# Kernel tuning notes

Measured on AMD Instinct MI355X. Metric: run time of the kernel, lower is better.

The kernel has to match this reference:

```python
import jax, jax.numpy as jnp
import numpy as np

B, L, E, H = 1, 4096, 1024, 16
D = E // H
EPS = 1e-6


def setup_inputs() -> dict:
    key = jax.random.key(0)
    k1, k2, k3 = jax.random.split(key, 3)
    # fan-in scaled init to keep activations sane
    x = jax.random.normal(k1, (B, L, E), dtype=jnp.float32)
    qkv_w = jax.random.normal(k2, (E, 3 * E), dtype=jnp.float32) / np.sqrt(E)
    qkv_b = jnp.zeros((3 * E,), dtype=jnp.float32)
    out_w = jax.random.normal(k3, (E, E), dtype=jnp.float32) / np.sqrt(E)
    out_b = jnp.zeros((E,), dtype=jnp.float32)
    return {"x": x, "qkv_w": qkv_w, "qkv_b": qkv_b, "out_w": out_w, "out_b": out_b}


def reference(x, qkv_w, qkv_b, out_w, out_b):
    b, l, e = x.shape
    qkv = x @ qkv_w + qkv_b                      # (B, L, 3E)
    q, k, v = jnp.split(qkv, 3, axis=-1)
    # (B, L, E) -> (B, H, L, D)
    q = q.reshape(b, l, H, D).transpose(0, 2, 1, 3)
    k = k.reshape(b, l, H, D).transpose(0, 2, 1, 3)
    v = v.reshape(b, l, H, D).transpose(0, 2, 1, 3)
    q_prime = jax.nn.elu(q) + 1.0
    k_prime = jax.nn.elu(k) + 1.0
    # cumulative sum of per-position outer products k'_l v_l^T : (B,H,L,D,D)
    kv_prod = jnp.einsum('bhld,bhle->bhlde', k_prime, v)
    kv_cumsum = jnp.cumsum(kv_prod, axis=2)
    context = jnp.einsum('bhld,bhlde->bhle', q_prime, kv_cumsum)  # (B,H,L,D)
    k_cumsum = jnp.cumsum(k_prime, axis=2)                        # (B,H,L,D)
    norm = jnp.einsum('bhld,bhld->bhl', q_prime, k_cumsum)        # (B,H,L)
    output = context / (norm[..., None] + EPS)
    output = output.transpose(0, 2, 1, 3).reshape(b, l, e)
    return output @ out_w + out_b
```

## Files before the change

kernel.cpp:

```cpp
#include <hip/hip_runtime.h>
#include <cstddef>
#include <cstdint>

#define L_SEQ 4096
#define EMB   1024
#define NH    16
#define HD    64
#define N3    3072
#define CHUNK 64
#define NCHUNK 64
#define EPS 1e-6f

typedef __attribute__((ext_vector_type(8))) short   bf16x8;
typedef __attribute__((ext_vector_type(4))) short   bf16x4;
typedef __attribute__((ext_vector_type(4))) float   floatx4;

#define AS1 __attribute__((address_space(1)))
#define AS3 __attribute__((address_space(3)))

__device__ __forceinline__ void gload_lds16(const void* g, void* l) {
    __builtin_amdgcn_global_load_lds((AS1 const unsigned int*)g,
                                     (AS3 unsigned int*)l, 16, 0, 0);
}

__device__ __forceinline__ short f2bf(float f) {
    union { float f; unsigned u; } a; a.f = f;
    unsigned r = a.u + 0x7fffu + ((a.u >> 16) & 1u);
    return (short)(r >> 16);
}
__device__ __forceinline__ float bf2f(short s) {
    union { unsigned u; float f; } a; a.u = ((unsigned)(unsigned short)s) << 16;
    return a.f;
}

__device__ __forceinline__ void transpose_tile(const float* __restrict__ W,
                                               short* __restrict__ WT,
                                               int K, int N, int bx, int by,
                                               float (*t)[65], int tid)
{
    const int r  = tid >> 4;
    const int c4 = (tid & 15) << 2;
#pragma unroll
    for (int s = 0; s < 4; ++s) {
        const int k = r + s * 16;
        const floatx4 v = *(const floatx4*)&W[(size_t)(by * 64 + k) * N + bx * 64 + c4];
        t[k][c4 + 0] = v[0]; t[k][c4 + 1] = v[1];
        t[k][c4 + 2] = v[2]; t[k][c4 + 3] = v[3];
    }
    __syncthreads();
#pragma unroll
    for (int s = 0; s < 4; ++s) {
        const int n = r + s * 16;
        bf16x4 o;
        o[0] = f2bf(t[c4 + 0][n]); o[1] = f2bf(t[c4 + 1][n]);
        o[2] = f2bf(t[c4 + 2][n]); o[3] = f2bf(t[c4 + 3][n]);
        *(bf16x4*)&WT[(size_t)(bx * 64 + n) * K + by * 64 + c4] = o;
    }
}

__global__ __launch_bounds__(256)
void prep(const float* __restrict__ x, short* __restrict__ xb,
          const float* __restrict__ qkv_w, short* __restrict__ qwt,
          const float* __restrict__ out_w, short* __restrict__ owt)
{
    __shared__ float t[64][65];
    const int b = blockIdx.x;
    const int tid = threadIdx.x;
    if (b < 2048) {
        const int i = b * 256 + tid;
        const floatx4 a = *(const floatx4*)(x + (size_t)i * 8);
        const floatx4 c = *(const floatx4*)(x + (size_t)i * 8 + 4);
        bf16x8 o;
        o[0] = f2bf(a[0]); o[1] = f2bf(a[1]); o[2] = f2bf(a[2]); o[3] = f2bf(a[3]);
        o[4] = f2bf(c[0]); o[5] = f2bf(c[1]); o[6] = f2bf(c[2]); o[7] = f2bf(c[3]);
        *(bf16x8*)(xb + (size_t)i * 8) = o;
    } else if (b < 2048 + 768) {
        const int u = b - 2048;
        transpose_tile(qkv_w, qwt, EMB, N3, u % 48, u / 48, t, tid);
    } else {
        const int u = b - 2816;
        transpose_tile(out_w, owt, EMB, EMB, u & 15, u >> 4, t, tid);
    }
}

#define CST 136

__global__ __launch_bounds__(256)
void mfma_gemm_qkv(const short* __restrict__ A, const short* __restrict__ BT,
                   const float* __restrict__ bias,
                   short* __restrict__ OQ, short* __restrict__ OK,
                   short* __restrict__ OV, int N, int K)
{
    __shared__ __align__(16) short smem[128 * CST];
    short* pan[4] = { smem, smem + 4096, smem + 8192, smem + 12288 };
    const int tid  = threadIdx.x;
    const int lane = tid & 63;
    const int wave = tid >> 6;
    const int wm = (wave >> 1) * 64;
    const int wn = (wave & 1) * 64;
    const int bx = blockIdx.x;
    const int by = blockIdx.y;
    const int frow = lane & 15;
    const int quad = lane >> 4;
    const int fko  = quad << 3;

    const short* Ab = A  + (size_t)(by * 128) * K;
    const short* Bb = BT + (size_t)(bx * 128) * K;

    floatx4 acc[4][4] = {};

    for (int k0 = 0; k0 < K; k0 += 64) {
#pragma unroll
        for (int p = 0; p < 2; ++p) {
            const int kp = k0 + p * 32;
#pragma unroll
            for (int q = 0; q < 2; ++q) {
                const int ia = q * 256 + tid;
                const int row = ia >> 2;
                const int kc  = (ia & 3) << 3;
                gload_lds16(Ab + (size_t)row * K + kp + kc, &pan[p * 2 + 0][ia << 3]);
                gload_lds16(Bb + (size_t)row * K + kp + kc, &pan[p * 2 + 1][ia << 3]);
            }
        }
        __syncthreads();
#pragma unroll
        for (int p = 0; p < 2; ++p) {
            bf16x8 af[4], bfv[4];
#pragma unroll
            for (int mi = 0; mi < 4; ++mi)
                af[mi] = *(const bf16x8*)&pan[p * 2 + 0][(wm + mi * 16 + frow) * 32 + fko];
#pragma unroll
            for (int ni = 0; ni < 4; ++ni)
                bfv[ni] = *(const bf16x8*)&pan[p * 2 + 1][(wn + ni * 16 + frow) * 32 + fko];
#pragma unroll
            for (int mi = 0; mi < 4; ++mi)
#pragma unroll
                for (int ni = 0; ni < 4; ++ni)
                    acc[mi][ni] = __builtin_amdgcn_mfma_f32_16x16x32_bf16(
                        af[mi], bfv[ni], acc[mi][ni], 0, 0, 0);
        }
        __syncthreads();
    }

    const int rq = quad << 2;
#pragma unroll
    for (int ni = 0; ni < 4; ++ni) {
        const int n = bx * 128 + wn + ni * 16 + frow;
        const float bv = bias[n];
        const bool do_elu = (n >> 10) < 2;
#pragma unroll
        for (int mi = 0; mi < 4; ++mi)
#pragma unroll
            for (int r = 0; r < 4; ++r) {
                float v = acc[mi][ni][r] + bv;
                if (do_elu) v = (v > 0.f) ? (v + 1.f) : __expf(v);
                smem[(wm + mi * 16 + rq + r) * CST + wn + ni * 16 + frow] = f2bf(v);
            }
    }
    __syncthreads();
#pragma unroll
    for (int t = 0; t < 8; ++t) {
        const int idx = t * 256 + tid;
        const int mm = idx >> 4;
        const int c8 = (idx & 15) << 3;
        const bf16x8 val = *(const bf16x8*)&smem[mm * CST + c8];
        const int n0 = bx * 128 + c8;
        const int rsel = n0 >> 10;
        const int h  = (n0 & 1023) >> 6;
        const int d  = n0 & 63;
        short* base = (rsel == 0) ? OQ : (rsel == 1 ? OK : OV);
        *(bf16x8*)&base[((size_t)(h * L_SEQ + by * 128 + mm)) * HD + d] = val;
    }
}

__global__ __launch_bounds__(256)
void mfma_gemm_out(const short* __restrict__ A, const short* __restrict__ BT,
                   const float* __restrict__ bias, float* __restrict__ OF,
                   int N, int K)
{
    __shared__ __align__(16) short smem[12288];
    short* pan[4] = { smem, smem + 2048, smem + 6144, smem + 8192 };
    const int tid  = threadIdx.x;
    const int lane = tid & 63;
    const int wave = tid >> 6;
    const int wm = (wave >> 1) * 32;
    const int wn = (wave & 1) * 64;
    const int bx = blockIdx.x;
    const int by = blockIdx.y;
    const int frow = lane & 15;
    const int quad = lane >> 4;
    const int fko  = quad << 3;

    const short* Ab = A  + (size_t)(by * 64) * K;
    const short* Bb = BT + (size_t)(bx * 128) * K;

    floatx4 acc[2][4] = {};

    for (int k0 = 0; k0 < K; k0 += 64) {
#pragma unroll
        for (int p = 0; p < 2; ++p) {
            const int kp = k0 + p * 32;
            {
                const int row = tid >> 2;
                const int kc  = (tid & 3) << 3;
                gload_lds16(Ab + (size_t)row * K + kp + kc, &pan[p * 2 + 0][tid << 3]);
            }
#pragma unroll
            for (int q = 0; q < 2; ++q) {
                const int ib = q * 256 + tid;
                const int row = ib >> 2;
                const int kc  = (ib & 3) << 3;
                gload_lds16(Bb + (size_t)row * K + kp + kc, &pan[p * 2 + 1][ib << 3]);
            }
        }
        __syncthreads();
#pragma unroll
        for (int p = 0; p < 2; ++p) {
            bf16x8 af[2], bfv[4];
#pragma unroll
            for (int mi = 0; mi < 2; ++mi)
                af[mi] = *(const bf16x8*)&pan[p * 2 + 0][(wm + mi * 16 + frow) * 32 + fko];
#pragma unroll
            for (int ni = 0; ni < 4; ++ni)
                bfv[ni] = *(const bf16x8*)&pan[p * 2 + 1][(wn + ni * 16 + frow) * 32 + fko];
#pragma unroll
            for (int mi = 0; mi < 2; ++mi)
#pragma unroll
                for (int ni = 0; ni < 4; ++ni)
                    acc[mi][ni] = __builtin_amdgcn_mfma_f32_16x16x32_bf16(
                        af[mi], bfv[ni], acc[mi][ni], 0, 0, 0);
        }
        __syncthreads();
    }

    const int rq = quad << 2;
#pragma unroll
    for (int ni = 0; ni < 4; ++ni) {
        const int n = bx * 128 + wn + ni * 16 + frow;
        const float bv = bias[n];
#pragma unroll
        for (int mi = 0; mi < 2; ++mi)
#pragma unroll
            for (int r = 0; r < 4; ++r) {
                const int m = by * 64 + wm + mi * 16 + rq + r;
                OF[(size_t)m * N + n] = acc[mi][ni][r] + bv;
            }
    }
}

#define SP 72

__global__ __launch_bounds__(256, 4)
void chunk_state(const short* __restrict__ Kb, const short* __restrict__ Vb,
                 short* __restrict__ ScTb, float* __restrict__ zc)
{
    __shared__ __align__(16) short Vt[64 * SP];
    __shared__ __align__(16) short Kt[64 * SP];
    const int c = blockIdx.x, h = blockIdx.y;
    const int tid = threadIdx.x, lane = tid & 63, wave = tid >> 6;
    const int frow = lane & 15;
    const int quad = lane >> 4;
    const int fko  = quad << 3;
    const int wm   = wave << 4;
    const short* Kg = Kb + ((size_t)h * L_SEQ + (size_t)c * CHUNK) * HD;
    const short* Vg = Vb + ((size_t)h * L_SEQ + (size_t)c * CHUNK) * HD;

#pragma unroll
    for (int q = 0; q < 2; ++q) {
        const int idx = q * 256 + tid;
        const int l = idx >> 3, c8 = (idx & 7) << 3;
        const bf16x8 vv = *(const bf16x8*)&Vg[l * 64 + c8];
        const bf16x8 kk = *(const bf16x8*)&Kg[l * 64 + c8];
#pragma unroll
        for (int j = 0; j < 8; ++j) {
            Vt[(c8 + j) * SP + l] = vv[j];
            Kt[(c8 + j) * SP + l] = kk[j];
        }
    }
    __syncthreads();

    const bf16x8 af0 = *(const bf16x8*)&Vt[(wm + frow) * SP + fko];
    const bf16x8 af1 = *(const bf16x8*)&Vt[(wm + frow) * SP + 32 + fko];

    floatx4 acc[4] = {};
#pragma unroll
    for (int n = 0; n < 4; ++n) {
        const bf16x8 kf0 = *(const bf16x8*)&Kt[(n * 16 + frow) * SP + fko];
        const bf16x8 kf1 = *(const bf16x8*)&Kt[(n * 16 + frow) * SP + 32 + fko];
        acc[n] = __builtin_amdgcn_mfma_f32_16x16x32_bf16(af0, kf0, acc[n], 0, 0, 0);
        acc[n] = __builtin_amdgcn_mfma_f32_16x16x32_bf16(af1, kf1, acc[n], 0, 0, 0);
    }

    short* Sout = ScTb + (size_t)(h * NCHUNK + c) * 4096;
#pragma unroll
    for (int n = 0; n < 4; ++n)
#pragma unroll
        for (int r = 0; r < 4; ++r) {
            const int e = wm + quad * 4 + r;
            const int d = n * 16 + frow;
            Sout[e * 64 + d] = f2bf(acc[n][r]);
        }

    if (wave == 0) {
        bf16x8 ones;
#pragma unroll
        for (int j = 0; j < 8; ++j) ones[j] = (short)0x3F80;
        floatx4 zacc[4] = {};
#pragma unroll
        for (int n = 0; n < 4; ++n) {
            const bf16x8 kf0 = *(const bf16x8*)&Kt[(n * 16 + frow) * SP + fko];
            const bf16x8 kf1 = *(const bf16x8*)&Kt[(n * 16 + frow) * SP + 32 + fko];
            zacc[n] = __builtin_amdgcn_mfma_f32_16x16x32_bf16(ones, kf0, zacc[n], 0, 0, 0);
            zacc[n] = __builtin_amdgcn_mfma_f32_16x16x32_bf16(ones, kf1, zacc[n], 0, 0, 0);
        }
        if (quad == 0) {
#pragma unroll
            for (int n = 0; n < 4; ++n)
                zc[(size_t)(h * NCHUNK + c) * 64 + n * 16 + frow] = zacc[n][0];
        }
    }
}

__global__ __launch_bounds__(256)
void prefix_scan(const short* __restrict__ ScTb, const float* __restrict__ zc,
                 short* __restrict__ S0b)
{
    const int g = blockIdx.x * 256 + threadIdx.x;
    const int h  = g >> 12;
    const int ed = g & 4095;
    const int e  = ed >> 6;
    const int d  = ed & 63;
    const short* src = ScTb + (size_t)h * NCHUNK * 4096 + ed;
    float run = 0.f;
    for (int cb = 0; cb < NCHUNK; cb += 8) {
        short v[8];
#pragma unroll
        for (int u = 0; u < 8; ++u) v[u] = src[(size_t)(cb + u) * 4096];
#pragma unroll
        for (int u = 0; u < 8; ++u) {
            S0b[((size_t)((h * NCHUNK + cb + u) * 65 + e)) * 64 + d] = f2bf(run);
            run += bf2f(v[u]);
        }
    }
    if (g < NH * HD) {
        const int h2 = g >> 6, d2 = g & 63;
        float rz = 0.f;
        for (int cb = 0; cb < NCHUNK; cb += 8) {
            float w[8];
#pragma unroll
            for (int u = 0; u < 8; ++u)
                w[u] = zc[((size_t)(h2 * NCHUNK + cb + u)) * HD + d2];
#pragma unroll
            for (int u = 0; u < 8; ++u) {
                S0b[((size_t)((h2 * NCHUNK + cb + u) * 65 + 64)) * 64 + d2] = f2bf(rz);
                rz += w[u];
            }
        }
    }
}

__global__ __launch_bounds__(256)
void chunk_attn(const short* __restrict__ Qb, const short* __restrict__ Kb,
                const short* __restrict__ Vb, const short* __restrict__ S0b,
                short* __restrict__ attn)
{
    __shared__ __align__(16) short Vs[65 * SP];
    __shared__ __align__(16) short As[64 * SP];
    const int c = blockIdx.x, h = blockIdx.y;
    const int tid = threadIdx.x, lane = tid & 63, wave = tid >> 6;
    const size_t rb = ((size_t)h * L_SEQ + (size_t)c * CHUNK) * HD;
    const short* Qg = Qb + rb;
    const short* Kg = Kb + rb;
    const short* Vg = Vb + rb;
    const short* Sg = S0b + (size_t)(h * NCHUNK + c) * 65 * 64;

#pragma unroll
    for (int q = 0; q < 2; ++q) {
        const int idx = q * 256 + tid;
        const int row = idx >> 3, c8 = (idx & 7) << 3;
        const bf16x8 vv = *(const bf16x8*)&Vg[row * 64 + c8];
#pragma unroll
        for (int j = 0; j < 8; ++j) Vs[(c8 + j) * SP + row] = vv[j];
    }
    if (tid < 64) Vs[64 * SP + tid] = (short)0x3F80;
    __syncthreads();

    const int frow = lane & 15;
    const int quad = lane >> 4;
    const int fko  = quad << 3;
    const int wm   = wave << 4;

    const bf16x8 qf0 = *(const bf16x8*)&Qg[(wm + frow) * 64 + fko];
    const bf16x8 qf1 = *(const bf16x8*)&Qg[(wm + frow) * 64 + 32 + fko];

    floatx4 sacc[4] = {};
#pragma unroll
    for (int n = 0; n < 4; ++n) {
        const bf16x8 kf0 = *(const bf16x8*)&Kg[(n * 16 + frow) * 64 + fko];
        const bf16x8 kf1 = *(const bf16x8*)&Kg[(n * 16 + frow) * 64 + 32 + fko];
        sacc[n] = __builtin_amdgcn_mfma_f32_16x16x32_bf16(qf0, kf0, sacc[n], 0, 0, 0);
        sacc[n] = __builtin_amdgcn_mfma_f32_16x16x32_bf16(qf1, kf1, sacc[n], 0, 0, 0);
    }
#pragma unroll
    for (int n = 0; n < 4; ++n)
#pragma unroll
        for (int r = 0; r < 4; ++r) {
            const int i = wm + quad * 4 + r;
            const int j = n * 16 + frow;
            As[i * SP + j] = (j <= i) ? f2bf(sacc[n][r]) : (short)0;
        }
    const bf16x8 af0 = *(const bf16x8*)&As[(wm + frow) * SP + fko];
    const bf16x8 af1 = *(const bf16x8*)&As[(wm + frow) * SP + 32 + fko];

    floatx4 oacc[5] = {};
#pragma unroll
    for (int n = 0; n < 4; ++n) {
        const bf16x8 vf0 = *(const bf16x8*)&Vs[(n * 16 + frow) * SP + fko];
        const bf16x8 vf1 = *(const bf16x8*)&Vs[(n * 16 + frow) * SP + 32 + fko];
        oacc[n] = __builtin_amdgcn_mfma_f32_16x16x32_bf16(af0, vf0, oacc[n], 0, 0, 0);
        oacc[n] = __builtin_amdgcn_mfma_f32_16x16x32_bf16(af1, vf1, oacc[n], 0, 0, 0);
        const bf16x8 sf0 = *(const bf16x8*)&Sg[(n * 16 + frow) * 64 + fko];
        const bf16x8 sf1 = *(const bf16x8*)&Sg[(n * 16 + frow) * 64 + 32 + fko];
        oacc[n] = __builtin_amdgcn_mfma_f32_16x16x32_bf16(qf0, sf0, oacc[n], 0, 0, 0);
        oacc[n] = __builtin_amdgcn_mfma_f32_16x16x32_bf16(qf1, sf1, oacc[n], 0, 0, 0);
    }
    {
        const bf16x8 vf0 = *(const bf16x8*)&Vs[64 * SP + fko];
        const bf16x8 vf1 = *(const bf16x8*)&Vs[64 * SP + 32 + fko];
        oacc[4] = __builtin_amdgcn_mfma_f32_16x16x32_bf16(af0, vf0, oacc[4], 0, 0, 0);
        oacc[4] = __builtin_amdgcn_mfma_f32_16x16x32_bf16(af1, vf1, oacc[4], 0, 0, 0);
        const bf16x8 sf0 = *(const bf16x8*)&Sg[64 * 64 + fko];
        const bf16x8 sf1 = *(const bf16x8*)&Sg[64 * 64 + 32 + fko];
        oacc[4] = __builtin_amdgcn_mfma_f32_16x16x32_bf16(qf0, sf0, oacc[4], 0, 0, 0);
        oacc[4] = __builtin_amdgcn_mfma_f32_16x16x32_bf16(qf1, sf1, oacc[4], 0, 0, 0);
    }
#pragma unroll
    for (int r = 0; r < 4; ++r) {
        const float norm = __shfl(oacc[4][r], lane & 48) + EPS;
        const float inv = 1.f / norm;
        const int i = wm + quad * 4 + r;
#pragma unroll
        for (int n = 0; n < 4; ++n)
            As[i * SP + n * 16 + frow] = f2bf(oacc[n][r] * inv);
    }
    __syncthreads();
#pragma unroll
    for (int t = 0; t < 2; ++t) {
        const int idx = t * 256 + tid;
        const int row = idx >> 3, c8 = (idx & 7) << 3;
        *(bf16x8*)&attn[(size_t)(c * CHUNK + row) * EMB + h * HD + c8] =
            *(const bf16x8*)&As[row * SP + c8];
    }
}

extern "C" void kernel_launch(void* const* d_in, const int* in_sizes, int n_in,
                              void* d_out, int out_size, void* d_ws, size_t ws_size,
                              hipStream_t stream)
{
    const float* x     = (const float*)d_in[0];
    const float* qkv_w = (const float*)d_in[1];
    const float* qkv_b = (const float*)d_in[2];
    const float* out_w = (const float*)d_in[3];
    const float* out_b = (const float*)d_in[4];
    float* out = (float*)d_out;

    short* ws    = (short*)d_ws;
    short* Qb    = ws;
    short* Kb    = Qb + 4194304;
    short* Vb    = Kb + 4194304;
    short* xb    = Vb + 4194304;
    short* qwt   = xb + 4194304;
    short* owt   = qwt + 3145728;
    short* attnb = owt + 1048576;
    short* ScTb  = attnb + 4194304;
    short* S0b   = ScTb + 4194304;
    float* zc    = (float*)(S0b + 4259840);

    prep<<<dim3(3072), 256, 0, stream>>>(x, xb, qkv_w, qwt, out_w, owt);
    mfma_gemm_qkv<<<dim3(N3 / 128, L_SEQ / 128), 256, 0, stream>>>(
        xb, qwt, qkv_b, Qb, Kb, Vb, N3, EMB);
    chunk_state<<<dim3(NCHUNK, NH), 256, 0, stream>>>(Kb, Vb, ScTb, zc);
    prefix_scan<<<dim3((NH * 4096) / 256), 256, 0, stream>>>(ScTb, zc, S0b);
    chunk_attn<<<dim3(NCHUNK, NH), 256, 0, stream>>>(Qb, Kb, Vb, S0b, attnb);
    mfma_gemm_out<<<dim3(EMB / 128, L_SEQ / 64), 256, 0, stream>>>(
        attnb, owt, out_b, out, EMB, EMB);
}
```

Measured before the change: 166.3 us.

## Rewrite QKV GEMM as 256x256 tile with swizzled LDS and phased prefetch pipeline

Replaces the 128x128, 256-thread QKV GEMM with a 256x256, 512-thread kernel that uses 128KB of LDS, an XOR-swizzled layout to avoid bank conflicts, and an 8-phase schedule. Each phase overlaps global-to-LDS staging of the next K slices with MFMA work, using explicit barriers, waitcnt and setprio. The aim is higher data reuse per tile and hidden load latency. The trade-off is only 12x16=192 blocks on a large GPU, which risks underfilling the CUs, plus heavy LDS use and fragile manual synchronisation.

Result: no change. 168.3 us (+1.2%).

```diff
diff --git a/kernel.cpp b/kernel.cpp
--- a/kernel.cpp
+++ b/kernel.cpp
@@ -83,94 +83,141 @@
     }
 }
 
-#define CST 136
-
-__global__ __launch_bounds__(256)
-void mfma_gemm_qkv(const short* __restrict__ A, const short* __restrict__ BT,
-                   const float* __restrict__ bias,
-                   short* __restrict__ OQ, short* __restrict__ OK,
-                   short* __restrict__ OV, int N, int K)
-{
-    __shared__ __align__(16) short smem[128 * CST];
-    short* pan[4] = { smem, smem + 4096, smem + 8192, smem + 12288 };
+#define MFMA16 __builtin_amdgcn_mfma_f32_16x16x32_bf16
+
+__global__ __launch_bounds__(512, 2)
+void mfma_gemm_qkv256(const short* __restrict__ A, const short* __restrict__ BT,
+                      const float* __restrict__ bias,
+                      short* __restrict__ OQ, short* __restrict__ OK,
+                      short* __restrict__ OV)
+{
+    __shared__ __align__(16) short lds[65536];
     const int tid  = threadIdx.x;
     const int lane = tid & 63;
     const int wave = tid >> 6;
-    const int wm = (wave >> 1) * 64;
-    const int wn = (wave & 1) * 64;
+    const int wr   = wave >> 2;
+    const int wc   = wave & 3;
+    const int frow = lane & 15;
+    const int quad = lane >> 4;
+    const int q8   = quad * 8;
     const int bx = blockIdx.x;
     const int by = blockIdx.y;
-    const int frow = lane & 15;
-    const int quad = lane >> 4;
-    const int fko  = quad << 3;
-
-    const short* Ab = A  + (size_t)(by * 128) * K;
-    const short* Bb = BT + (size_t)(bx * 128) * K;
-
-    floatx4 acc[4][4] = {};
-
-    for (int k0 = 0; k0 < K; k0 += 64) {
-#pragma unroll
-        for (int p = 0; p < 2; ++p) {
-            const int kp = k0 + p * 32;
-#pragma unroll
-            for (int q = 0; q < 2; ++q) {
-                const int ia = q * 256 + tid;
-                const int row = ia >> 2;
-                const int kc  = (ia & 3) << 3;
-                gload_lds16(Ab + (size_t)row * K + kp + kc, &pan[p * 2 + 0][ia << 3]);
-                gload_lds16(Bb + (size_t)row * K + kp + kc, &pan[p * 2 + 1][ia << 3]);
-            }
-        }
-        __syncthreads();
-#pragma unroll
-        for (int p = 0; p < 2; ++p) {
-            bf16x8 af[4], bfv[4];
-#pragma unroll
-            for (int mi = 0; mi < 4; ++mi)
-                af[mi] = *(const bf16x8*)&pan[p * 2 + 0][(wm + mi * 16 + frow) * 32 + fko];
-#pragma unroll
-            for (int ni = 0; ni < 4; ++ni)
-                bfv[ni] = *(const bf16x8*)&pan[p * 2 + 1][(wn + ni * 16 + frow) * 32 + fko];
-#pragma unroll
-            for (int mi = 0; mi < 4; ++mi)
-#pragma unroll
-                for (int ni = 0; ni < 4; ++ni)
-                    acc[mi][ni] = __builtin_amdgcn_mfma_f32_16x16x32_bf16(
-                        af[mi], bfv[ni], acc[mi][ni], 0, 0, 0);
-        }
-        __syncthreads();
-    }
-
-    const int rq = quad << 2;
+
+    const short* Ab = A  + (size_t)(by * 256) * 1024;
+    const short* Bb = BT + (size_t)(bx * 256) * 1024;
+
+    const int trow = tid >> 3;
+    const int ccol = (tid & 7) * 8;
+    const int scol = ccol ^ ((trow & 12) << 2);
+    const int sx = (frow & 12) << 2;
+    const int wcb = wc * 64 + frow;
+
+#define STG(LBASE, GPTR) do {                                               \
+        const short* g_ = (GPTR);                                           \
+        _Pragma("unroll")                                                   \
+        for (int j_ = 0; j_ < 2; ++j_) {                                    \
+            const int r_ = j_ * 64 + trow;                                  \
+            gload_lds16(g_ + (size_t)r_ * 1024 + scol,                      \
+                        &lds[(LBASE) + r_ * 64 + ccol]);                    \
+        }                                                                   \
+    } while (0)
+
+#define LDA(BASE, R, KS) \
+    (*(const bf16x8*)&lds[(BASE) + (R) * 64 + ((((KS) * 32) + q8) ^ sx)])
+
+    floatx4 acc[8][4] = {};
+    bf16x8  bq[4][2];
+
+#define PHASE(ABASE, BBASE, QD, RDB, VM, ...) do {                          \
+        const int Rr_ = wr * 128 + (QD) * 32 + frow;                        \
+        bf16x8 a0_ = LDA((ABASE), Rr_,      0);                             \
+        bf16x8 a1_ = LDA((ABASE), Rr_,      1);                             \
+        bf16x8 a2_ = LDA((ABASE), Rr_ + 16, 0);                             \
+        bf16x8 a3_ = LDA((ABASE), Rr_ + 16, 1);                             \
+        if (RDB) {                                                          \
+            _Pragma("unroll")                                               \
+            for (int ni_ = 0; ni_ < 4; ++ni_) {                             \
+                bq[ni_][0] = LDA((BBASE), wcb + ni_ * 16, 0);               \
+                bq[ni_][1] = LDA((BBASE), wcb + ni_ * 16, 1);               \
+            }                                                               \
+        }                                                                   \
+        __VA_ARGS__;                                                        \
+        __builtin_amdgcn_sched_barrier(0);                                  \
+        __builtin_amdgcn_s_barrier();                                       \
+        asm volatile("s_waitcnt lgkmcnt(0)" ::: "memory");                  \
+        __builtin_amdgcn_sched_barrier(0);                                  \
+        __builtin_amdgcn_s_setprio(1);                                      \
+        _Pragma("unroll")                                                   \
+        for (int ni_ = 0; ni_ < 4; ++ni_) {                                 \
+            acc[2*(QD)  ][ni_] = MFMA16(a0_, bq[ni_][0], acc[2*(QD)  ][ni_], 0,0,0); \
+            acc[2*(QD)  ][ni_] = MFMA16(a1_, bq[ni_][1], acc[2*(QD)  ][ni_], 0,0,0); \
+            acc[2*(QD)+1][ni_] = MFMA16(a2_, bq[ni_][0], acc[2*(QD)+1][ni_], 0,0,0); \
+            acc[2*(QD)+1][ni_] = MFMA16(a3_, bq[ni_][1], acc[2*(QD)+1][ni_], 0,0,0); \
+        }                                                                   \
+        __builtin_amdgcn_s_setprio(0);                                      \
+        if (VM) asm volatile("s_waitcnt vmcnt(4)" ::: "memory");            \
+        __builtin_amdgcn_s_barrier();                                       \
+        __builtin_amdgcn_sched_barrier(0);                                  \
+    } while (0)
+
+    STG(0,     Ab);
+    STG(8192,  Ab + 131072);
+    STG(16384, Bb);
+    STG(24576, Bb + 131072);
+    STG(49152, Bb + 64);
+    STG(57344, Bb + 131072 + 64);
+    asm volatile("s_waitcnt vmcnt(4)" ::: "memory");
+    __builtin_amdgcn_s_barrier();
+    __builtin_amdgcn_sched_barrier(0);
+
+#pragma unroll 1
+    for (int it = 0; it < 8; ++it) {
+        const int k1  = (2 * it + 1) * 64;
+        const int kn0 = ((2 * it + 2) & 15) * 64;
+        const int kn1 = ((2 * it + 3) & 15) * 64;
+
+        PHASE(0, 16384, 0, 1, 0,
+              STG(32768, Ab + k1); STG(40960, Ab + 131072 + k1));
+        PHASE(0, 16384, 1, 0, 0, STG(16384, Bb + kn0));
+        PHASE(0, 16384, 2, 0, 0, STG(24576, Bb + 131072 + kn0));
+        PHASE(0, 16384, 3, 0, 1, ((void)0));
+        PHASE(32768, 49152, 0, 1, 0, STG(0,    Ab + kn0));
+        PHASE(32768, 49152, 1, 0, 0, STG(8192, Ab + 131072 + kn0));
+        PHASE(32768, 49152, 2, 0, 0, STG(49152, Bb + kn1));
+        PHASE(32768, 49152, 3, 0, 1, STG(57344, Bb + 131072 + kn1));
+    }
+
+    __syncthreads();
+
+    const int wbase = wave * 8192;
+    const int colg0 = bx * 256 + wc * 64;
+    const int rsel  = colg0 >> 10;
+    const bool do_elu = rsel < 2;
+    short* obase = (rsel == 0) ? OQ : (rsel == 1 ? OK : OV);
+    const int h  = (colg0 >> 6) & 15;
+    const int L0 = by * 256 + wr * 128;
 #pragma unroll
     for (int ni = 0; ni < 4; ++ni) {
-        const int n = bx * 128 + wn + ni * 16 + frow;
-        const float bv = bias[n];
-        const bool do_elu = (n >> 10) < 2;
-#pragma unroll
-        for (int mi = 0; mi < 4; ++mi)
+        const float bv = bias[colg0 + ni * 16 + frow];
+#pragma unroll
+        for (int mi = 0; mi < 8; ++mi)
 #pragma unroll
             for (int r = 0; r < 4; ++r) {
                 float v = acc[mi][ni][r] + bv;
                 if (do_elu) v = (v > 0.f) ? (v + 1.f) : __expf(v);
-                smem[(wm + mi * 16 + rq + r) * CST + wn + ni * 16 + frow] = f2bf(v);
+                lds[wbase + (mi * 16 + quad * 4 + r) * 64 + ni * 16 + frow] = f2bf(v);
             }
     }
-    __syncthreads();
-#pragma unroll
-    for (int t = 0; t < 8; ++t) {
-        const int idx = t * 256 + tid;
-        const int mm = idx >> 4;
-        const int c8 = (idx & 15) << 3;
-        const bf16x8 val = *(const bf16x8*)&smem[mm * CST + c8];
-        const int n0 = bx * 128 + c8;
-        const int rsel = n0 >> 10;
-        const int h  = (n0 & 1023) >> 6;
-        const int d  = n0 & 63;
-        short* base = (rsel == 0) ? OQ : (rsel == 1 ? OK : OV);
-        *(bf16x8*)&base[((size_t)(h * L_SEQ + by * 128 + mm)) * HD + d] = val;
-    }
+#pragma unroll
+    for (int s = 0; s < 16; ++s) {
+        const int chunk = s * 64 + lane;
+        const int row = chunk >> 3, c8 = (chunk & 7) * 8;
+        *(bf16x8*)&obase[((size_t)(h * L_SEQ + L0 + row)) * HD + c8] =
+            *(const bf16x8*)&lds[wbase + row * 64 + c8];
+    }
+#undef PHASE
+#undef LDA
+#undef STG
 }
 
 __global__ __launch_bounds__(256)
@@ -477,8 +524,8 @@
     float* zc    = (float*)(S0b + 4259840);
 
     prep<<<dim3(3072), 256, 0, stream>>>(x, xb, qkv_w, qwt, out_w, owt);
-    mfma_gemm_qkv<<<dim3(N3 / 128, L_SEQ / 128), 256, 0, stream>>>(
-        xb, qwt, qkv_b, Qb, Kb, Vb, N3, EMB);
+    mfma_gemm_qkv256<<<dim3(N3 / 256, L_SEQ / 256), 512, 0, stream>>>(
+        xb, qwt, qkv_b, Qb, Kb, Vb);
     chunk_state<<<dim3(NCHUNK, NH), 256, 0, stream>>>(Kb, Vb, ScTb, zc);
     prefix_scan<<<dim3((NH * 4096) / 256), 256, 0, stream>>>(ScTb, zc, S0b);
     chunk_attn<<<dim3(NCHUNK, NH), 256, 0, stream>>>(Qb, Kb, Vb, S0b, attnb);
```
